# Kernel tuning notes

Measured on AMD Instinct MI355X. Metric: run time of the kernel, lower is better.

Reference implementation:

```python
import jax, jax.numpy as jnp
import numpy as np

NEG = -1e12  # additive causal mask value used in the original TF code


def setup_inputs() -> dict:
    key = jax.random.key(0)
    k1, k2, k3, k4 = jax.random.split(key, 4)
    B, T, D, U = 4, 4096, 128, 128
    query = jax.random.normal(k1, (B, T, D), dtype=jnp.float32)
    # glorot-style scaled dense weights (no bias, matching use_bias=False)
    s = 1.0 / np.sqrt(D)
    Wq = jax.random.normal(k2, (D, U), dtype=jnp.float32) * s
    Wk = jax.random.normal(k3, (D, U), dtype=jnp.float32) * s
    Wv = jax.random.normal(k4, (D, U), dtype=jnp.float32) * s
    return {"query": query, "Wq": Wq, "Wk": Wk, "Wv": Wv}


def reference(query, Wq, Wk, Wv):
    # Self-attention path: value = key = query (pre-projection)
    q = jnp.einsum('btd,du->btu', query, Wq)
    k = jnp.einsum('btd,du->btu', query, Wk)
    v = jnp.einsum('btd,du->btu', query, Wv)
    T = v.shape[1]
    # NOTE: original scales by sqrt(seq_len) (tf.shape(value)[1]), kept faithfully
    scores = jnp.einsum('bqu,bku->bqk', q, k) / jnp.sqrt(jnp.asarray(T, jnp.float32))
    # additive causal mask: lower-triangular kept, upper gets -1e12
    causal = jnp.tril(jnp.ones((T, T), dtype=jnp.float32))
    scores = scores + NEG * (1.0 - causal)
    attn = jax.nn.softmax(scores, axis=-1)
    context = jnp.einsum('bqk,bku->bqu', attn, v)
    return context
```

## Files before the change

kernel.cpp:

```cpp
#include <hip/hip_runtime.h>

#define T_SEQ 4096
#define BATCH 4
#define DD 128
#define BT (BATCH * T_SEQ)

typedef __bf16 bf16x8 __attribute__((ext_vector_type(8)));
typedef float f32x4 __attribute__((ext_vector_type(4)));

__device__ inline bf16x8 ld8(const unsigned short* p) {
  return *reinterpret_cast<const bf16x8*>(p);
}
__device__ inline unsigned short bfc(float f) {
  __bf16 v = (__bf16)f;
  return __builtin_bit_cast(unsigned short, v);
}

#define MFMA(a, b, c) __builtin_amdgcn_mfma_f32_16x16x32_bf16((a), (b), (c), 0, 0, 0)

__global__ void wt_kernel(const float* __restrict__ Wq, const float* __restrict__ Wk,
                          const float* __restrict__ Wv,
                          unsigned short* __restrict__ fq, unsigned short* __restrict__ fk,
                          unsigned short* __restrict__ fv) {
  const float* W = (blockIdx.y == 0) ? Wq : (blockIdx.y == 1) ? Wk : Wv;
  unsigned short* F = (blockIdx.y == 0) ? fq : (blockIdx.y == 1) ? fk : fv;
  int e = blockIdx.x * 256 + threadIdx.x;
  int j = e & 7, lane = (e >> 3) & 63, nc = e >> 9;
  int c = nc & 3, n0 = nc >> 2;
  int t = lane & 15, g = lane >> 4;
  F[e] = bfc(W[(c * 32 + g * 8 + j) * 128 + n0 * 16 + t]);
}

__global__ __launch_bounds__(256) void proj_kernel(
    const float* __restrict__ X,
    const unsigned short* __restrict__ fq,
    const unsigned short* __restrict__ fk,
    const unsigned short* __restrict__ fv,
    unsigned short* __restrict__ qf,
    unsigned short* __restrict__ kf,
    unsigned short* __restrict__ vt) {
  const int tid = threadIdx.x;
  const int w = tid >> 6, lane = tid & 63;
  const int t = lane & 15, g = lane >> 4;
  const int r0 = blockIdx.x * 32;

  __shared__ unsigned short xs[2][16 * 136];

  bf16x8 wq[2][4], wk[2][4], wv[2][4];
#pragma unroll
  for (int s = 0; s < 2; ++s)
#pragma unroll
    for (int c = 0; c < 4; ++c) {
      int fo = (((w + s * 4) * 4 + c) * 64 + lane) * 8;
      wq[s][c] = ld8(fq + fo);
      wk[s][c] = ld8(fk + fo);
      wv[s][c] = ld8(fv + fo);
    }

#pragma unroll
  for (int sub = 0; sub < 2; ++sub) {
    int r = tid >> 4, cb = tid & 15;
    const float* xp = X + (size_t)(r0 + sub * 16 + r) * DD + cb * 8;
    float4 lo = *reinterpret_cast<const float4*>(xp);
    float4 hi = *reinterpret_cast<const float4*>(xp + 4);
    bf16x8 tmp;
    tmp[0] = (__bf16)lo.x; tmp[1] = (__bf16)lo.y; tmp[2] = (__bf16)lo.z; tmp[3] = (__bf16)lo.w;
    tmp[4] = (__bf16)hi.x; tmp[5] = (__bf16)hi.y; tmp[6] = (__bf16)hi.z; tmp[7] = (__bf16)hi.w;
    *reinterpret_cast<bf16x8*>(&xs[sub][r * 136 + cb * 8]) = tmp;
  }
  __syncthreads();

#pragma unroll
  for (int sub = 0; sub < 2; ++sub) {
    const int r0s = r0 + sub * 16;
    bf16x8 x[4];
#pragma unroll
    for (int c = 0; c < 4; ++c)
      x[c] = ld8(&xs[sub][t * 136 + c * 32 + g * 8]);

#pragma unroll
    for (int s = 0; s < 2; ++s) {
      const int n0 = w + s * 4;
      f32x4 aq = {0.f, 0.f, 0.f, 0.f}, ak = {0.f, 0.f, 0.f, 0.f};
#pragma unroll
      for (int c = 0; c < 4; ++c) {
        aq = MFMA(x[c], wq[s][c], aq);
        ak = MFMA(x[c], wk[s][c], ak);
      }
      const int cP = n0 >> 1;
      const int Gp = ((n0 & 1) << 1) | (t >> 3);
      const int ep = t & 7;
#pragma unroll
      for (int r = 0; r < 4; ++r) {
        int row = r0s + g * 4 + r;
        size_t qoff = ((size_t)((row >> 4) * 4 + cP) * 64 + ((Gp << 4) | (row & 15))) * 8 + ep;
        qf[qoff] = bfc(aq[r] * 0.015625f);
        int tp = (row & 3) | (((row >> 3) & 3) << 2);
        size_t koff =
            ((size_t)(((row >> 5) * 2 + ((row >> 2) & 1)) * 4 + cP) * 64 + ((Gp << 4) | tp)) * 8 +
            ep;
        kf[koff] = bfc(ak[r]);
      }
    }

    const int key = r0s + t;
    const size_t vbase = (size_t)(key >> 5) * 4096 + (key & 31);
#pragma unroll
    for (int s = 0; s < 2; ++s) {
      const int u0 = w + s * 4;
      f32x4 av = {0.f, 0.f, 0.f, 0.f};
#pragma unroll
      for (int c = 0; c < 4; ++c)
        av = MFMA(wv[s][c], x[c], av);
#pragma unroll
      for (int r = 0; r < 4; ++r)
        vt[vbase + (size_t)(u0 * 16 + g * 4 + r) * 32] = bfc(av[r]);
    }
  }
}

__global__ __launch_bounds__(256, 2) void attn_kernel(
    const unsigned short* __restrict__ qf,
    const unsigned short* __restrict__ kf,
    const unsigned short* __restrict__ vt,
    float* __restrict__ out) {
  const int tid = threadIdx.x;
  const int w = tid >> 6, lane = tid & 63;
  const int t = lane & 15, G = lane >> 4;
  const int bi = blockIdx.x;
  const int xcd = bi & 7;
  const int b = xcd >> 1;
  const int wi = ((bi >> 3) << 1) | (xcd & 1);
  const int sigma = 127 - wi;
  const int q0 = sigma * 32;
  const int nch = sigma + 1;

  const unsigned short* kfb = kf + (size_t)b * 128 * 4096;
  const unsigned short* vtb = vt + (size_t)b * 128 * 4096;

  bf16x8 qa[2][4];
#pragma unroll
  for (int p = 0; p < 2; ++p)
#pragma unroll
    for (int c = 0; c < 4; ++c)
      qa[p][c] = ld8(qf + ((size_t)((b * 256 + 2 * sigma + p) * 4 + c) * 64 + lane) * 8);

  f32x4 O[2][8];
#pragma unroll
  for (int p = 0; p < 2; ++p)
#pragma unroll
    for (int u0 = 0; u0 < 8; ++u0) O[p][u0] = (f32x4){0.f, 0.f, 0.f, 0.f};
  float ls0 = 0.f, ls1 = 0.f;

  int j = w;
  bf16x8 kcur[8];
  if (j < nch) {
    const unsigned short* kblk = kfb + (size_t)j * 4096;
#pragma unroll
    for (int ci = 0; ci < 8; ++ci) kcur[ci] = ld8(kblk + ci * 512 + lane * 8);
  }

  for (; j < nch; j += 4) {
    const int j0 = j * 32;
    const unsigned short* vblk = vtb + (size_t)j * 4096;
    bf16x8 vcur[8];
#pragma unroll
    for (int u0 = 0; u0 < 8; ++u0) vcur[u0] = ld8(vblk + (u0 * 16 + t) * 32 + G * 8);
    bf16x8 knxt[8];
    if (j + 4 < nch) {
      const unsigned short* kb2 = kfb + (size_t)(j + 4) * 4096;
#pragma unroll
      for (int ci = 0; ci < 8; ++ci) knxt[ci] = ld8(kb2 + ci * 512 + lane * 8);
    }

    f32x4 s00 = (f32x4){0.f, 0.f, 0.f, 0.f}, s01 = (f32x4){0.f, 0.f, 0.f, 0.f};
    f32x4 s10 = (f32x4){0.f, 0.f, 0.f, 0.f}, s11 = (f32x4){0.f, 0.f, 0.f, 0.f};
#pragma unroll
    for (int c = 0; c < 4; ++c) {
      s00 = MFMA(kcur[c], qa[0][c], s00);
      s01 = MFMA(kcur[4 + c], qa[0][c], s01);
      s10 = MFMA(kcur[c], qa[1][c], s10);
      s11 = MFMA(kcur[4 + c], qa[1][c], s11);
    }

    bf16x8 pb0, pb1;
#pragma unroll
    for (int r = 0; r < 4; ++r) {
      int k0 = j0 + G * 8 + r;
      float e00 = (k0 <= q0 + t) ? __expf(s00[r]) : 0.f;
      float e01 = (k0 + 4 <= q0 + t) ? __expf(s01[r]) : 0.f;
      float e10 = (k0 <= q0 + 16 + t) ? __expf(s10[r]) : 0.f;
      float e11 = (k0 + 4 <= q0 + 16 + t) ? __expf(s11[r]) : 0.f;
      ls0 += e00 + e01;
      ls1 += e10 + e11;
      pb0[r] = (__bf16)e00; pb0[r + 4] = (__bf16)e01;
      pb1[r] = (__bf16)e10; pb1[r + 4] = (__bf16)e11;
    }

#pragma unroll
    for (int u0 = 0; u0 < 8; ++u0) {
      O[0][u0] = MFMA(pb0, vcur[u0], O[0][u0]);
      O[1][u0] = MFMA(pb1, vcur[u0], O[1][u0]);
    }
#pragma unroll
    for (int ci = 0; ci < 8; ++ci) kcur[ci] = knxt[ci];
  }

  __shared__ float cmb[3][64][66];
  if (w > 0) {
#pragma unroll
    for (int p = 0; p < 2; ++p)
#pragma unroll
      for (int u0 = 0; u0 < 8; ++u0)
        *reinterpret_cast<f32x4*>(&cmb[w - 1][lane][p * 32 + u0 * 4]) = O[p][u0];
    cmb[w - 1][lane][64] = ls0;
    cmb[w - 1][lane][65] = ls1;
  }
  __syncthreads();
  if (w == 0) {
#pragma unroll
    for (int ww = 0; ww < 3; ++ww) {
#pragma unroll
      for (int p = 0; p < 2; ++p)
#pragma unroll
        for (int u0 = 0; u0 < 8; ++u0) {
          f32x4 q4 = *reinterpret_cast<const f32x4*>(&cmb[ww][lane][p * 32 + u0 * 4]);
          O[p][u0][0] += q4[0]; O[p][u0][1] += q4[1];
          O[p][u0][2] += q4[2]; O[p][u0][3] += q4[3];
        }
      ls0 += cmb[ww][lane][64];
      ls1 += cmb[ww][lane][65];
    }
    ls0 += __shfl_xor(ls0, 16); ls0 += __shfl_xor(ls0, 32);
    ls1 += __shfl_xor(ls1, 16); ls1 += __shfl_xor(ls1, 32);
    float linv0[4], linv1[4];
#pragma unroll
    for (int r = 0; r < 4; ++r) {
      linv0[r] = 1.0f / __shfl(ls0, G * 4 + r);
      linv1[r] = 1.0f / __shfl(ls1, G * 4 + r);
    }
    float* op0 = out + ((size_t)(b * T_SEQ + q0 + G * 4)) * DD + t;
    float* op1 = op0 + (size_t)16 * DD;
#pragma unroll
    for (int u0 = 0; u0 < 8; ++u0) {
#pragma unroll
      for (int r = 0; r < 4; ++r) {
        op0[(size_t)r * DD + u0 * 16] = O[0][u0][r] * linv0[r];
        op1[(size_t)r * DD + u0 * 16] = O[1][u0][r] * linv1[r];
      }
    }
  }
}

extern "C" void kernel_launch(void* const* d_in, const int* in_sizes, int n_in,
                              void* d_out, int out_size, void* d_ws, size_t ws_size,
                              hipStream_t stream) {
  const float* X  = (const float*)d_in[0];
  const float* Wq = (const float*)d_in[1];
  const float* Wk = (const float*)d_in[2];
  const float* Wv = (const float*)d_in[3];
  float* out = (float*)d_out;

  unsigned short* qf = (unsigned short*)d_ws;
  unsigned short* kf = qf + (size_t)BT * DD;
  unsigned short* vt = kf + (size_t)BT * DD;
  unsigned short* fq = vt + (size_t)BT * DD;
  unsigned short* fk = fq + DD * DD;
  unsigned short* fv = fk + DD * DD;

  dim3 wt_grid(64, 3);
  wt_kernel<<<wt_grid, 256, 0, stream>>>(Wq, Wk, Wv, fq, fk, fv);
  proj_kernel<<<BT / 32, 256, 0, stream>>>(X, fq, fk, fv, qf, kf, vt);
  attn_kernel<<<512, 256, 0, stream>>>(qf, kf, vt, out);
}
```

Baseline: 112.2 us.

## Double query tile per block, swizzle V layout for coalesced loads, skip mask on interior chunks

```diff
diff --git a/kernel.cpp b/kernel.cpp
--- a/kernel.cpp
+++ b/kernel.cpp
@@ -104,7 +104,8 @@
     }
 
     const int key = r0s + t;
-    const size_t vbase = (size_t)(key >> 5) * 4096 + (key & 31);
+    const int kk = key & 31;
+    const size_t vbase = (size_t)(key >> 5) * 4096 + (size_t)(kk >> 3) * 128 + (kk & 7);
 #pragma unroll
     for (int s = 0; s < 2; ++s) {
       const int u0 = w + s * 4;
@@ -114,12 +115,12 @@
         av = MFMA(wv[s][c], x[c], av);
 #pragma unroll
       for (int r = 0; r < 4; ++r)
-        vt[vbase + (size_t)(u0 * 16 + g * 4 + r) * 32] = bfc(av[r]);
-    }
-  }
-}
-
-__global__ __launch_bounds__(256, 2) void attn_kernel(
+        vt[vbase + (size_t)u0 * 512 + (g * 4 + r) * 8] = bfc(av[r]);
+    }
+  }
+}
+
+__global__ __launch_bounds__(256, 1) void attn_kernel(
     const unsigned short* __restrict__ qf,
     const unsigned short* __restrict__ kf,
     const unsigned short* __restrict__ vt,
@@ -131,123 +132,144 @@
   const int xcd = bi & 7;
   const int b = xcd >> 1;
   const int wi = ((bi >> 3) << 1) | (xcd & 1);
-  const int sigma = 127 - wi;
-  const int q0 = sigma * 32;
-  const int nch = sigma + 1;
+  const int gamma = 63 - wi;
+  const int q0 = gamma * 64;
+  const int nch = 2 * gamma + 2;
 
   const unsigned short* kfb = kf + (size_t)b * 128 * 4096;
   const unsigned short* vtb = vt + (size_t)b * 128 * 4096;
 
-  bf16x8 qa[2][4];
-#pragma unroll
-  for (int p = 0; p < 2; ++p)
+  bf16x8 qa[4][4];
+#pragma unroll
+  for (int p = 0; p < 4; ++p)
 #pragma unroll
     for (int c = 0; c < 4; ++c)
-      qa[p][c] = ld8(qf + ((size_t)((b * 256 + 2 * sigma + p) * 4 + c) * 64 + lane) * 8);
-
-  f32x4 O[2][8];
-#pragma unroll
-  for (int p = 0; p < 2; ++p)
+      qa[p][c] = ld8(qf + ((size_t)((b * 256 + 4 * gamma + p) * 4 + c) * 64 + lane) * 8);
+
+  f32x4 O[4][8];
+#pragma unroll
+  for (int p = 0; p < 4; ++p)
 #pragma unroll
     for (int u0 = 0; u0 < 8; ++u0) O[p][u0] = (f32x4){0.f, 0.f, 0.f, 0.f};
-  float ls0 = 0.f, ls1 = 0.f;
+  float ls[4] = {0.f, 0.f, 0.f, 0.f};
 
   int j = w;
-  bf16x8 kcur[8];
+  bf16x8 kc[8], vc[8];
   if (j < nch) {
     const unsigned short* kblk = kfb + (size_t)j * 4096;
-#pragma unroll
-    for (int ci = 0; ci < 8; ++ci) kcur[ci] = ld8(kblk + ci * 512 + lane * 8);
+    const unsigned short* vblk = vtb + (size_t)j * 4096;
+#pragma unroll
+    for (int ci = 0; ci < 8; ++ci) {
+      kc[ci] = ld8(kblk + ci * 512 + lane * 8);
+      vc[ci] = ld8(vblk + ci * 512 + lane * 8);
+    }
   }
 
   for (; j < nch; j += 4) {
+    const bool hn = (j + 4) < nch;
+    bf16x8 kn[8], vn[8];
+    if (hn) {
+      const unsigned short* kb2 = kfb + (size_t)(j + 4) * 4096;
+      const unsigned short* vb2 = vtb + (size_t)(j + 4) * 4096;
+#pragma unroll
+      for (int ci = 0; ci < 8; ++ci) {
+        kn[ci] = ld8(kb2 + ci * 512 + lane * 8);
+        vn[ci] = ld8(vb2 + ci * 512 + lane * 8);
+      }
+    }
+
+    f32x4 s0[4], s1[4];
+#pragma unroll
+    for (int p = 0; p < 4; ++p) {
+      s0[p] = (f32x4){0.f, 0.f, 0.f, 0.f};
+      s1[p] = (f32x4){0.f, 0.f, 0.f, 0.f};
+    }
+#pragma unroll
+    for (int c = 0; c < 4; ++c)
+#pragma unroll
+      for (int p = 0; p < 4; ++p) {
+        s0[p] = MFMA(kc[c], qa[p][c], s0[p]);
+        s1[p] = MFMA(kc[4 + c], qa[p][c], s1[p]);
+      }
+
     const int j0 = j * 32;
-    const unsigned short* vblk = vtb + (size_t)j * 4096;
-    bf16x8 vcur[8];
-#pragma unroll
-    for (int u0 = 0; u0 < 8; ++u0) vcur[u0] = ld8(vblk + (u0 * 16 + t) * 32 + G * 8);
-    bf16x8 knxt[8];
-    if (j + 4 < nch) {
-      const unsigned short* kb2 = kfb + (size_t)(j + 4) * 4096;
-#pragma unroll
-      for (int ci = 0; ci < 8; ++ci) knxt[ci] = ld8(kb2 + ci * 512 + lane * 8);
-    }
-
-    f32x4 s00 = (f32x4){0.f, 0.f, 0.f, 0.f}, s01 = (f32x4){0.f, 0.f, 0.f, 0.f};
-    f32x4 s10 = (f32x4){0.f, 0.f, 0.f, 0.f}, s11 = (f32x4){0.f, 0.f, 0.f, 0.f};
-#pragma unroll
-    for (int c = 0; c < 4; ++c) {
-      s00 = MFMA(kcur[c], qa[0][c], s00);
-      s01 = MFMA(kcur[4 + c], qa[0][c], s01);
-      s10 = MFMA(kcur[c], qa[1][c], s10);
-      s11 = MFMA(kcur[4 + c], qa[1][c], s11);
-    }
-
-    bf16x8 pb0, pb1;
-#pragma unroll
-    for (int r = 0; r < 4; ++r) {
-      int k0 = j0 + G * 8 + r;
-      float e00 = (k0 <= q0 + t) ? __expf(s00[r]) : 0.f;
-      float e01 = (k0 + 4 <= q0 + t) ? __expf(s01[r]) : 0.f;
-      float e10 = (k0 <= q0 + 16 + t) ? __expf(s10[r]) : 0.f;
-      float e11 = (k0 + 4 <= q0 + 16 + t) ? __expf(s11[r]) : 0.f;
-      ls0 += e00 + e01;
-      ls1 += e10 + e11;
-      pb0[r] = (__bf16)e00; pb0[r + 4] = (__bf16)e01;
-      pb1[r] = (__bf16)e10; pb1[r + 4] = (__bf16)e11;
-    }
-
-#pragma unroll
-    for (int u0 = 0; u0 < 8; ++u0) {
-      O[0][u0] = MFMA(pb0, vcur[u0], O[0][u0]);
-      O[1][u0] = MFMA(pb1, vcur[u0], O[1][u0]);
-    }
-#pragma unroll
-    for (int ci = 0; ci < 8; ++ci) kcur[ci] = knxt[ci];
-  }
-
-  __shared__ float cmb[3][64][66];
-  if (w > 0) {
-#pragma unroll
-    for (int p = 0; p < 2; ++p)
+    bf16x8 pb[4];
+    if (j < 2 * gamma) {
+#pragma unroll
+      for (int p = 0; p < 4; ++p)
+#pragma unroll
+        for (int r = 0; r < 4; ++r) {
+          float e0 = __expf(s0[p][r]);
+          float e1 = __expf(s1[p][r]);
+          ls[p] += e0 + e1;
+          pb[p][r] = (__bf16)e0;
+          pb[p][r + 4] = (__bf16)e1;
+        }
+    } else {
+#pragma unroll
+      for (int p = 0; p < 4; ++p) {
+        const int lim = q0 + p * 16 + t;
+#pragma unroll
+        for (int r = 0; r < 4; ++r) {
+          int k0 = j0 + G * 8 + r;
+          float e0 = (k0 <= lim) ? __expf(s0[p][r]) : 0.f;
+          float e1 = (k0 + 4 <= lim) ? __expf(s1[p][r]) : 0.f;
+          ls[p] += e0 + e1;
+          pb[p][r] = (__bf16)e0;
+          pb[p][r + 4] = (__bf16)e1;
+        }
+      }
+    }
+
+#pragma unroll
+    for (int u0 = 0; u0 < 8; ++u0)
+#pragma unroll
+      for (int p = 0; p < 4; ++p)
+        O[p][u0] = MFMA(pb[p], vc[u0], O[p][u0]);
+
+    if (hn) {
+#pragma unroll
+      for (int ci = 0; ci < 8; ++ci) { kc[ci] = kn[ci]; vc[ci] = vn[ci]; }
+    }
+  }
+
+  __shared__ float cmb[3][64][36];
+#pragma unroll 1
+  for (int p = 0; p < 4; ++p) {
+    __syncthreads();
+    if (w > 0) {
 #pragma unroll
       for (int u0 = 0; u0 < 8; ++u0)
-        *reinterpret_cast<f32x4*>(&cmb[w - 1][lane][p * 32 + u0 * 4]) = O[p][u0];
-    cmb[w - 1][lane][64] = ls0;
-    cmb[w - 1][lane][65] = ls1;
-  }
-  __syncthreads();
-  if (w == 0) {
-#pragma unroll
-    for (int ww = 0; ww < 3; ++ww) {
-#pragma unroll
-      for (int p = 0; p < 2; ++p)
+        *reinterpret_cast<f32x4*>(&cmb[w - 1][lane][u0 * 4]) = O[p][u0];
+      cmb[w - 1][lane][32] = ls[p];
+    }
+    __syncthreads();
+    if (w == 0) {
+      f32x4 acc[8];
+#pragma unroll
+      for (int u0 = 0; u0 < 8; ++u0) acc[u0] = O[p][u0];
+      float lt = ls[p];
+#pragma unroll
+      for (int ww = 0; ww < 3; ++ww) {
 #pragma unroll
         for (int u0 = 0; u0 < 8; ++u0) {
-          f32x4 q4 = *reinterpret_cast<const f32x4*>(&cmb[ww][lane][p * 32 + u0 * 4]);
-          O[p][u0][0] += q4[0]; O[p][u0][1] += q4[1];
-          O[p][u0][2] += q4[2]; O[p][u0][3] += q4[3];
+          f32x4 q4 = *reinterpret_cast<const f32x4*>(&cmb[ww][lane][u0 * 4]);
+          acc[u0][0] += q4[0]; acc[u0][1] += q4[1];
+          acc[u0][2] += q4[2]; acc[u0][3] += q4[3];
         }
-      ls0 += cmb[ww][lane][64];
-      ls1 += cmb[ww][lane][65];
-    }
-    ls0 += __shfl_xor(ls0, 16); ls0 += __shfl_xor(ls0, 32);
-    ls1 += __shfl_xor(ls1, 16); ls1 += __shfl_xor(ls1, 32);
-    float linv0[4], linv1[4];
-#pragma unroll
-    for (int r = 0; r < 4; ++r) {
-      linv0[r] = 1.0f / __shfl(ls0, G * 4 + r);
-      linv1[r] = 1.0f / __shfl(ls1, G * 4 + r);
-    }
-    float* op0 = out + ((size_t)(b * T_SEQ + q0 + G * 4)) * DD + t;
-    float* op1 = op0 + (size_t)16 * DD;
-#pragma unroll
-    for (int u0 = 0; u0 < 8; ++u0) {
-#pragma unroll
-      for (int r = 0; r < 4; ++r) {
-        op0[(size_t)r * DD + u0 * 16] = O[0][u0][r] * linv0[r];
-        op1[(size_t)r * DD + u0 * 16] = O[1][u0][r] * linv1[r];
-      }
+        lt += cmb[ww][lane][32];
+      }
+      lt += __shfl_xor(lt, 16);
+      lt += __shfl_xor(lt, 32);
+      float linv[4];
+#pragma unroll
+      for (int r = 0; r < 4; ++r) linv[r] = 1.0f / __shfl(lt, G * 4 + r);
+      float* op = out + ((size_t)(b * T_SEQ + q0 + p * 16 + G * 4)) * DD + t;
+#pragma unroll
+      for (int u0 = 0; u0 < 8; ++u0)
+#pragma unroll
+        for (int r = 0; r < 4; ++r)
+          op[(size_t)r * DD + u0 * 16] = acc[u0][r] * linv[r];
     }
   }
 }
@@ -271,5 +293,5 @@
   dim3 wt_grid(64, 3);
   wt_kernel<<<wt_grid, 256, 0, stream>>>(Wq, Wk, Wv, fq, fk, fv);
   proj_kernel<<<BT / 32, 256, 0, stream>>>(X, fq, fk, fv, qf, kf, vt);
-  attn_kernel<<<512, 256, 0, stream>>>(qf, kf, vt, out);
-}
+  attn_kernel<<<256, 256, 0, stream>>>(qf, kf, vt, out);
+}
```

New measurement: 128.1 us. +14.2%, slower.
